# Kernel tuning notes

Measured on AMD Instinct MI355X. Metric: run time of the kernel, lower is better.

Reference implementation:

```python
import jax, jax.numpy as jnp
import numpy as np
import math

D = 1024
H = 16
DH = D // H
B = 4
NSEQ = 1024
NSEG = 2
EXP = 4


def layer_norm(x, w, b=None, eps=1e-5):
    mu = jnp.mean(x, axis=-1, keepdims=True)
    var = jnp.mean((x - mu) ** 2, axis=-1, keepdims=True)
    y = (x - mu) * jax.lax.rsqrt(var + eps) * w
    return y + b if b is not None else y


def apply_rope(x, positions):
    # x: [B, L, H, Dh]; ESM-style rotate-half RoPE
    dh = x.shape[-1]
    inv_freq = 1.0 / (10000.0 ** (jnp.arange(0, dh, 2, dtype=jnp.float32) / dh))
    freqs = positions.astype(jnp.float32)[:, None] * inv_freq[None, :]  # [L, Dh/2]
    emb = jnp.concatenate([freqs, freqs], axis=-1)  # [L, Dh]
    cos = jnp.cos(emb)[None, :, None, :]
    sin = jnp.sin(emb)[None, :, None, :]
    x1, x2 = jnp.split(x, 2, axis=-1)
    return x * cos + jnp.concatenate([-x2, x1], axis=-1) * sin


def timestep_embedding(timesteps, embedding_dim=256, max_len=10000):
    # timesteps: [N]
    ts = timesteps * max_len
    half = embedding_dim // 2
    emb = math.log(max_len) / (half - 1)
    freqs = jnp.exp(jnp.arange(half, dtype=jnp.float32) * -emb)
    e = ts.astype(jnp.float32)[:, None] * freqs[None, :]
    return jnp.concatenate([jnp.sin(e), jnp.cos(e)], axis=1)  # [N, 256]


def make_autoregressive_attn_mask(batch_mask, n_seg):
    b, n_res = batch_mask.shape
    L = (n_seg + 1) * n_res
    causal = jnp.tril(jnp.ones((L, L), dtype=bool))[None, None]  # [1,1,L,L]
    tiled = jnp.tile(batch_mask, (1, n_seg + 1)).astype(bool)  # [B, L]
    key_valid = tiled[:, None, None, :]
    q_valid = tiled[:, None, :, None]
    allowed = causal & key_valid & q_valid  # [B,1,L,L]
    first_edit = (batch_mask[:, None, :] * batch_mask[:, :, None]).astype(bool)
    allowed = allowed.at[:, 0, :n_res, :n_res].set(first_edit)
    return allowed


def setup_inputs() -> dict:
    key = jax.random.key(0)
    ks = jax.random.split(key, 32)
    s = 0.02
    p = lambda i, shape: jax.random.normal(ks[i], shape, dtype=jnp.float32) * s
    inp = {
        'x_seq': jax.random.normal(ks[0], (B, NSEQ, D), dtype=jnp.float32),
        'x_struc': jax.random.normal(ks[1], (B, 1, D), dtype=jnp.float32),
        'temp': jax.random.uniform(ks[2], (B, 1, 1), dtype=jnp.float32),
        'mask': jnp.ones((B, NSEQ), dtype=jnp.float32),
        'ln_qs_w': jnp.ones((D,), jnp.float32), 'ln_qs_b': jnp.zeros((D,), jnp.float32),
        'W_qkv_seq': p(3, (D, 3 * D)),
        'ln_qt_w': jnp.ones((D,), jnp.float32), 'ln_qt_b': jnp.zeros((D,), jnp.float32),
        'W_qkv_struc': p(4, (D, 3 * D)),
        'q_ln_seq_w': jnp.ones((D,), jnp.float32), 'k_ln_seq_w': jnp.ones((D,), jnp.float32),
        'q_ln_struc_w': jnp.ones((D,), jnp.float32), 'k_ln_struc_w': jnp.ones((D,), jnp.float32),
        'W_out_seq': p(5, (D, D)), 'W_out_struc': p(6, (D, D)),
        'temp_w1': p(7, (1, D)), 'temp_b1': jnp.zeros((D,), jnp.float32),
        'temp_w2': p(8, (D, D)), 'temp_b2': jnp.zeros((D,), jnp.float32),
        'T_w1': p(9, (256, D)), 'T_b1': jnp.zeros((D,), jnp.float32),
        'T_w2': p(10, (D, D)), 'T_b2': jnp.zeros((D,), jnp.float32),
        'ffn_seq_ln_w': jnp.ones((D,), jnp.float32), 'ffn_seq_ln_b': jnp.zeros((D,), jnp.float32),
        'ffn_seq_w1': p(11, (D, EXP * D)), 'ffn_seq_w2': p(12, (EXP * D, D)),
        'ffn_struc_ln_w': jnp.ones((D,), jnp.float32), 'ffn_struc_ln_b': jnp.zeros((D,), jnp.float32),
        'ffn_struc_w1': p(13, (D, EXP * D)), 'ffn_struc_w2': p(14, (EXP * D, D)),
        'T': 1,
    }
    return inp


def reference(x_seq, x_struc, temp, mask,
              ln_qs_w, ln_qs_b, W_qkv_seq,
              ln_qt_w, ln_qt_b, W_qkv_struc,
              q_ln_seq_w, k_ln_seq_w, q_ln_struc_w, k_ln_struc_w,
              W_out_seq, W_out_struc,
              temp_w1, temp_b1, temp_w2, temp_b2,
              T_w1, T_b1, T_w2, T_b2,
              ffn_seq_ln_w, ffn_seq_ln_b, ffn_seq_w1, ffn_seq_w2,
              ffn_struc_ln_w, ffn_struc_ln_b, ffn_struc_w1, ffn_struc_w2,
              T):
    b, n_seq, d = x_seq.shape
    n_seg, index = NSEG, 0  # index=0 prefill path

    # --- seq track QKV (index == 0 only) ---
    qkv_seq = layer_norm(x_seq, ln_qs_w, ln_qs_b) @ W_qkv_seq
    q_s, k_s, v_s = jnp.split(qkv_seq, 3, axis=-1)
    q_s = layer_norm(q_s, q_ln_seq_w)
    k_s = layer_norm(k_s, k_ln_seq_w)
    pos_seq = jnp.arange(n_seq)
    q_s = apply_rope(q_s.reshape(b, n_seq, H, DH), pos_seq).reshape(b, n_seq, d)
    k_s = apply_rope(k_s.reshape(b, n_seq, H, DH), pos_seq).reshape(b, n_seq, d)

    # --- struc track conditioning + QKV ---
    position_T = jnp.arange(n_seg, dtype=jnp.float32) * T / 100.0
    T_input = jnp.repeat(position_T, n_seq)[index:index + 1]  # [1]
    x_norm = layer_norm(x_struc, ln_qt_w, ln_qt_b)
    temp_e = jax.nn.silu(temp @ temp_w1 + temp_b1) @ temp_w2 + temp_b2  # [B,1,D]
    t_emb = timestep_embedding(T_input)  # [1,256]
    T_e = jax.nn.silu(t_emb @ T_w1 + T_b1) @ T_w2 + T_b2  # [1,D]
    x_mod = x_norm + temp_e + T_e[None, :, :]
    qkv_t = x_mod @ W_qkv_struc
    q_t, k_t, v_t = jnp.split(qkv_t, 3, axis=-1)
    q_t = layer_norm(q_t, q_ln_struc_w)
    k_t = layer_norm(k_t, k_ln_struc_w)
    pos_res = jnp.tile(jnp.arange(n_seq), n_seg)[index:index + 1]  # [1]
    q_t = apply_rope(q_t.reshape(b, 1, H, DH), pos_res).reshape(b, 1, d)
    k_t = apply_rope(k_t.reshape(b, 1, H, DH), pos_res).reshape(b, 1, d)

    # --- KV cache contents for index 0: [seq tokens, struc token] ---
    keys = jnp.concatenate([k_s, k_t], axis=1)    # [B, N_seq+1, D]
    values = jnp.concatenate([v_s, v_t], axis=1)
    queries = jnp.concatenate([q_s, q_t], axis=1)

    to_heads = lambda t: t.reshape(b, -1, H, DH).transpose(0, 2, 1, 3)  # b h s d
    qh, kh, vh = to_heads(queries), to_heads(keys), to_heads(values)

    allowed = make_autoregressive_attn_mask(mask, n_seg)  # [B,1,L,L]
    Lq = n_seq + index + 1
    attn_mask = allowed[:, :, :Lq, :Lq]

    scale = 1.0 / math.sqrt(DH)
    scores = jnp.einsum('bhqd,bhkd->bhqk', qh, kh) * scale
    scores = jnp.where(attn_mask, scores, -1e9)
    probs = jax.nn.softmax(scores, axis=-1)
    ctx = jnp.einsum('bhqk,bhkd->bhqd', probs, vh)
    ctx = ctx.transpose(0, 2, 1, 3).reshape(b, Lq, d)

    out_seq = ctx[:, :n_seq] @ W_out_seq
    out_struc = ctx[:, n_seq:] @ W_out_struc

    # residuals (scaling_factor = 1)
    x_seq = x_seq + out_seq
    x_struc = x_struc + out_struc

    # GELU FFNs (LN -> Linear -> GELU -> Linear, no bias)
    h_seq = jax.nn.gelu(layer_norm(x_seq, ffn_seq_ln_w, ffn_seq_ln_b) @ ffn_seq_w1, approximate=False) @ ffn_seq_w2
    x_seq = x_seq + h_seq
    h_struc = jax.nn.gelu(layer_norm(x_struc, ffn_struc_ln_w, ffn_struc_ln_b) @ ffn_struc_w1, approximate=False) @ ffn_struc_w2
    x_struc = x_struc + h_struc

    return (x_seq, x_struc)
```

## Files before the change

### kernel.cpp

```cpp
#include <hip/hip_runtime.h>

typedef __attribute__((ext_vector_type(8))) short short8;
typedef __attribute__((ext_vector_type(4))) float f32x4;
typedef __attribute__((ext_vector_type(4))) unsigned short us4;

#define DEV static __device__ __forceinline__

DEV float bf2f(unsigned short u){ union{unsigned u; float f;} v; v.u=((unsigned)u)<<16; return v.f; }
DEV unsigned short f2bf(float f){ union{float f; unsigned u;} v; v.f=f; unsigned r=v.u+0x7fffu+((v.u>>16)&1u); return (unsigned short)(r>>16); }
DEV float gelu_f(float x){ return 0.5f*x*(1.0f+erff(x*0.7071067811865475f)); }
DEV float silu_f(float x){ return x/(1.0f+__expf(-x)); }

DEV void gload16(const void* g, void* l){
  __builtin_amdgcn_global_load_lds((const __attribute__((address_space(1))) void*)g,
                                   (__attribute__((address_space(3))) void*)l, 16, 0, 0);
}

DEV void blk_reduce2(float &a, float &b){
  #pragma unroll
  for (int off=32; off>0; off>>=1){ a += __shfl_down(a,off); b += __shfl_down(b,off); }
  __shared__ float sa[4], sb[4];
  int w=threadIdx.x>>6;
  if((threadIdx.x&63)==0){ sa[w]=a; sb[w]=b; }
  __syncthreads();
  a=sa[0]+sa[1]+sa[2]+sa[3]; b=sb[0]+sb[1]+sb[2]+sb[3];
}

template<int OUTF32>
__global__ __launch_bounds__(256) void ln_rows(const float* __restrict__ x,
    const float* __restrict__ w, const float* __restrict__ bias, void* __restrict__ outp)
{
  int row=blockIdx.x, t=threadIdx.x;
  const float* xr = x + (size_t)row*1024;
  float4 v = *(const float4*)(xr + t*4);
  float s=v.x+v.y+v.z+v.w;
  float s2=v.x*v.x+v.y*v.y+v.z*v.z+v.w*v.w;
  blk_reduce2(s,s2);
  float mu=s*(1.0f/1024.0f);
  float rs=rsqrtf(s2*(1.0f/1024.0f)-mu*mu+1e-5f);
  int d0=t*4;
  const float* vp=(const float*)&v;
  float y[4];
  #pragma unroll
  for(int j=0;j<4;j++){ float bb = bias? bias[d0+j] : 0.0f; y[j]=(vp[j]-mu)*rs*w[d0+j]+bb; }
  if (OUTF32){
    float4 o; o.x=y[0];o.y=y[1];o.z=y[2];o.w=y[3];
    *(float4*)((float*)outp + (size_t)row*1024 + d0) = o;
  } else {
    us4 o;
    #pragma unroll
    for(int j=0;j<4;j++) o[j]=f2bf(y[j]);
    *(us4*)((unsigned short*)outp + (size_t)row*1024 + d0) = o;
  }
}

__global__ __launch_bounds__(256) void wtrans(const float* __restrict__ Bm,
    unsigned short* __restrict__ Bt, int K, int N)
{
  __shared__ float tile[32][33];
  int nb = blockIdx.x*32, kb = blockIdx.y*32;
  int tx = threadIdx.x&31, ty = threadIdx.x>>5;
  #pragma unroll
  for(int i=0;i<32;i+=8) tile[ty+i][tx] = Bm[(size_t)(kb+ty+i)*N + nb+tx];
  __syncthreads();
  #pragma unroll
  for(int i=0;i<32;i+=8) Bt[(size_t)(nb+ty+i)*K + kb+tx] = f2bf(tile[tx][ty+i]);
}

__global__ void rope_table(float* __restrict__ tab){
  int idx = blockIdx.x*256 + threadIdx.x;
  if (idx >= 1024*32) return;
  int pos = idx>>5, i = idx&31;
  float inv = exp2f(-(float)i * (13.287712379549449f/32.0f));
  float a = (float)pos*inv;
  tab[idx*2]   = cosf(a);
  tab[idx*2+1] = sinf(a);
}

__global__ __launch_bounds__(256) void qk_ln_rope(
    const unsigned short* __restrict__ qkv, const float* __restrict__ qw, const float* __restrict__ kw,
    const float* __restrict__ tab, unsigned short* __restrict__ qr, unsigned short* __restrict__ kr)
{
  __shared__ float lnr[1024];
  int row=blockIdx.x, part=blockIdx.y, t=threadIdx.x;
  const unsigned short* src = qkv + (size_t)row*3072 + part*1024 + t*4;
  us4 u = *(const us4*)src;
  float x[4];
  #pragma unroll
  for(int j=0;j<4;j++) x[j]=bf2f(u[j]);
  float s=x[0]+x[1]+x[2]+x[3];
  float s2=x[0]*x[0]+x[1]*x[1]+x[2]*x[2]+x[3]*x[3];
  blk_reduce2(s,s2);
  float mu=s*(1.0f/1024.0f);
  float rsg=rsqrtf(s2*(1.0f/1024.0f)-mu*mu+1e-5f);
  const float* w = part? kw : qw;
  int d0=t*4;
  #pragma unroll
  for(int j=0;j<4;j++) lnr[d0+j]=(x[j]-mu)*rsg*w[d0+j];
  __syncthreads();
  int n = row & 1023;
  unsigned short* dst = (part? kr: qr) + (size_t)row*1024 + d0;
  us4 o;
  #pragma unroll
  for(int j=0;j<4;j++){
    int d=d0+j, dh=d&63, fi=dh&31;
    float c=tab[(n*32+fi)*2], sn=tab[(n*32+fi)*2+1];
    float p=lnr[d^32];
    o[j]=f2bf(lnr[d]*c + ((dh<32)? -p : p)*sn);
  }
  *(us4*)dst = o;
}

template<int EPI>
__global__ __launch_bounds__(256) void gemm_bt(
    const unsigned short* __restrict__ A, int lda,
    const unsigned short* __restrict__ Bt, int ldb,
    int N, int K, void* Cout, const float* resp)
{
  __shared__ unsigned short As[8192];
  __shared__ unsigned short Bs[8192];
  const int t=threadIdx.x;
  int GX=gridDim.x, GY=gridDim.y, nwg=GX*GY;
  int m0, n0;
  if (!((GX&7) || (nwg&63))){
    int d = blockIdx.y*GX + blockIdx.x;
    int xcd = d&7, j = d>>3;
    int g = xcd*(nwg>>3) + j;
    int chunk = g>>6, local = g&63;
    int chunks_x = GX>>3;
    int cx = chunk%chunks_x, cy = chunk/chunks_x;
    n0 = (cx*8 + (local&7))*128;
    m0 = (cy*8 + (local>>3))*128;
  } else {
    m0 = blockIdx.y*128; n0 = blockIdx.x*128;
  }
  const int kofs = blockIdx.z*K;
  const int l=t&63, w=t>>6, lg=l>>4, lr=l&15;
  const int wm=(w>>1)*64, wn=(w&1)*64;
  const int srow=t>>3, sseg=(t&7)^(srow&7);
  const f32x4 z4 = {0.f,0.f,0.f,0.f};
  f32x4 acc[4][4];
  #pragma unroll
  for(int i=0;i<4;i++)
    #pragma unroll
    for(int j=0;j<4;j++) acc[i][j]=z4;
  for (int k0=0;k0<K;k0+=64){
    __syncthreads();
    #pragma unroll
    for(int i=0;i<4;i++){
      gload16(A  + (size_t)(m0+srow+i*32)*lda + kofs + k0 + sseg*8, As + w*512 + i*2048);
      gload16(Bt + (size_t)(n0+srow+i*32)*ldb + kofs + k0 + sseg*8, Bs + w*512 + i*2048);
    }
    __syncthreads();
    #pragma unroll
    for(int ks=0;ks<2;ks++){
      short8 a[4], bfr[4];
      #pragma unroll
      for(int m=0;m<4;m++){
        int row=wm+m*16+lr;
        a[m] = *(const short8*)&As[row*64 + ((ks*4+lg)^(row&7))*8];
      }
      #pragma unroll
      for(int n=0;n<4;n++){
        int row=wn+n*16+lr;
        bfr[n] = *(const short8*)&Bs[row*64 + ((ks*4+lg)^(row&7))*8];
      }
      #pragma unroll
      for(int m=0;m<4;m++)
        #pragma unroll
        for(int n=0;n<4;n++)
          acc[m][n] = __builtin_amdgcn_mfma_f32_16x16x32_bf16(a[m], bfr[n], acc[m][n], 0,0,0);
    }
  }
  #pragma unroll
  for(int m=0;m<4;m++){
    #pragma unroll
    for(int n=0;n<4;n++){
      #pragma unroll
      for(int r=0;r<4;r++){
        int row=m0+wm+m*16+lg*4+r, col=n0+wn+n*16+lr;
        size_t idx=(size_t)row*N+col;
        float v=acc[m][n][r];
        if (EPI==1){ ((float*)Cout)[idx] = v + resp[idx]; }
        else if (EPI==2){ ((unsigned short*)Cout)[idx] = f2bf(gelu_f(v)); }
        else if (EPI==3){ atomicAdd((float*)Cout + idx, v); }
        else { ((unsigned short*)Cout)[idx] = f2bf(v); }
      }
    }
  }
}

__global__ __launch_bounds__(256) void flash_seq(
    const unsigned short* __restrict__ qr, const unsigned short* __restrict__ kr,
    const unsigned short* __restrict__ qkv, unsigned short* __restrict__ ctx)
{
  __shared__ unsigned short Kt[64][72];
  __shared__ unsigned short Vt[64][72];
  __shared__ unsigned short Pl[4][32][72];
  const int t=threadIdx.x, w=t>>6, l=t&63, lg=l>>4, lr=l&15;
  const int bh=blockIdx.y, b=bh>>4, h=bh&15;
  const int q0=blockIdx.x*128;
  const f32x4 z4 = {0.f,0.f,0.f,0.f};
  short8 qf[2][2];
  #pragma unroll
  for(int mf=0;mf<2;mf++)
    #pragma unroll
    for(int ks=0;ks<2;ks++)
      qf[mf][ks] = *(const short8*)(qr + (size_t)(b*1024 + q0 + w*32 + mf*16 + lr)*1024 + h*64 + ks*32 + lg*8);
  f32x4 o[2][4];
  float m_[2][4], l_[2][4];
  #pragma unroll
  for(int mf=0;mf<2;mf++){
    #pragma unroll
    for(int nd=0;nd<4;nd++) o[mf][nd]=z4;
    #pragma unroll
    for(int r=0;r<4;r++){ m_[mf][r]=-1e30f; l_[mf][r]=0.f; }
  }
  for (int kv0=0;kv0<1024;kv0+=64){
    __syncthreads();
    #pragma unroll
    for(int i=0;i<2;i++){
      int idx=t+i*256, rr=idx>>3, seg=idx&7;
      *(short8*)&Kt[rr][seg*8] = *(const short8*)(kr + (size_t)(b*1024+kv0+rr)*1024 + h*64 + seg*8);
    }
    #pragma unroll
    for(int i=0;i<2;i++){
      int idx=t+i*256, rr=idx>>3, seg=idx&7;
      short8 vv = *(const short8*)(qkv + (size_t)(b*1024+kv0+rr)*3072 + 2048 + h*64 + seg*8);
      #pragma unroll
      for(int j=0;j<8;j++) Vt[seg*8+j][rr] = (unsigned short)vv[j];
    }
    __syncthreads();
    f32x4 s[2][4];
    #pragma unroll
    for(int mf=0;mf<2;mf++)
      #pragma unroll
      for(int nf=0;nf<4;nf++) s[mf][nf]=z4;
    #pragma unroll
    for(int ks=0;ks<2;ks++){
      #pragma unroll
      for(int nf=0;nf<4;nf++){
        short8 kf = *(const short8*)&Kt[nf*16+lr][ks*32+lg*8];
        s[0][nf] = __builtin_amdgcn_mfma_f32_16x16x32_bf16(qf[0][ks], kf, s[0][nf],0,0,0);
        s[1][nf] = __builtin_amdgcn_mfma_f32_16x16x32_bf16(qf[1][ks], kf, s[1][nf],0,0,0);
      }
    }
    #pragma unroll
    for(int mf=0;mf<2;mf++)
      #pragma unroll
      for(int nf=0;nf<4;nf++) s[mf][nf] = s[mf][nf]*0.125f;
    #pragma unroll
    for(int mf=0;mf<2;mf++){
      #pragma unroll
      for(int r=0;r<4;r++){
        float mx = fmaxf(fmaxf(s[mf][0][r],s[mf][1][r]),fmaxf(s[mf][2][r],s[mf][3][r]));
        #pragma unroll
        for(int off=8;off>0;off>>=1) mx = fmaxf(mx, __shfl_xor(mx,off));
        float mn = fmaxf(m_[mf][r], mx);
        float f  = __expf(m_[mf][r]-mn);
        float rs = 0.f;
        #pragma unroll
        for(int nf=0;nf<4;nf++){ float p=__expf(s[mf][nf][r]-mn); s[mf][nf][r]=p; rs+=p; }
        #pragma unroll
        for(int off=8;off>0;off>>=1) rs += __shfl_xor(rs,off);
        l_[mf][r]=l_[mf][r]*f+rs; m_[mf][r]=mn;
        #pragma unroll
        for(int nd=0;nd<4;nd++) o[mf][nd][r]*=f;
      }
    }
    #pragma unroll
    for(int mf=0;mf<2;mf++)
      #pragma unroll
      for(int nf=0;nf<4;nf++)
        #pragma unroll
        for(int r=0;r<4;r++)
          Pl[w][mf*16+lg*4+r][nf*16+lr] = f2bf(s[mf][nf][r]);
    #pragma unroll
    for(int ks2=0;ks2<2;ks2++){
      short8 pa0 = *(const short8*)&Pl[w][lr]   [ks2*32+lg*8];
      short8 pa1 = *(const short8*)&Pl[w][16+lr][ks2*32+lg*8];
      #pragma unroll
      for(int nd=0;nd<4;nd++){
        short8 vf = *(const short8*)&Vt[nd*16+lr][ks2*32+lg*8];
        o[0][nd] = __builtin_amdgcn_mfma_f32_16x16x32_bf16(pa0, vf, o[0][nd],0,0,0);
        o[1][nd] = __builtin_amdgcn_mfma_f32_16x16x32_bf16(pa1, vf, o[1][nd],0,0,0);
      }
    }
  }
  #pragma unroll
  for(int mf=0;mf<2;mf++){
    #pragma unroll
    for(int r=0;r<4;r++){
      float inv = 1.0f/l_[mf][r];
      #pragma unroll
      for(int nd=0;nd<4;nd++){
        ctx[(size_t)(b*1024 + q0 + w*32 + mf*16 + lg*4 + r)*1024 + h*64 + nd*16 + lr]
          = f2bf(o[mf][nd][r]*inv);
      }
    }
  }
}

__global__ __launch_bounds__(256) void struc_prep_a(const float* __restrict__ T_w1, float* __restrict__ sTacc){
  int j = blockIdx.x*256+threadIdx.x;
  float u=0.f;
  #pragma unroll
  for(int i=0;i<16;i++) u += T_w1[(size_t)(128+blockIdx.y*16+i)*1024 + j];
  atomicAdd(&sTacc[j], u);
}

__global__ __launch_bounds__(256) void struc_prep_b(const float* __restrict__ temp,
    const float* __restrict__ temp_w1, const float* __restrict__ temp_b1,
    const float* __restrict__ T_b1, const float* __restrict__ sTacc,
    float* __restrict__ sT, float* __restrict__ stemp)
{
  int j = blockIdx.x*256+threadIdx.x;
  sT[j] = silu_f(sTacc[j]+T_b1[j]);
  #pragma unroll
  for(int b=0;b<4;b++){ float z = temp[b]*temp_w1[j]+temp_b1[j]; stemp[b*1024+j]=silu_f(z); }
}

__global__ __launch_bounds__(256) void struc_xmod(const float* __restrict__ xs,
    const float* __restrict__ qtw, const float* __restrict__ qtb,
    const float* __restrict__ eacc, const float* __restrict__ tacc,
    const float* __restrict__ temp_b2, const float* __restrict__ T_b2, float* __restrict__ xmod)
{
  int b=blockIdx.x, t=threadIdx.x;
  float4 v = *(const float4*)(xs + (size_t)b*1024 + t*4);
  float s=v.x+v.y+v.z+v.w, s2=v.x*v.x+v.y*v.y+v.z*v.z+v.w*v.w;
  blk_reduce2(s,s2);
  float mu=s*(1.0f/1024.0f);
  float rs=rsqrtf(s2*(1.0f/1024.0f)-mu*mu+1e-5f);
  const float* vp=(const float*)&v;
  #pragma unroll
  for(int j=0;j<4;j++){
    int d=t*4+j;
    xmod[b*1024+d] = (vp[j]-mu)*rs*qtw[d] + qtb[d] + eacc[b*1024+d] + tacc[d] + T_b2[d] + temp_b2[d];
  }
}

template<int MR>
__global__ __launch_bounds__(256) void smallm_part(
    const float* __restrict__ A, const float* __restrict__ Bm,
    float* __restrict__ accp, int K, int N)
{
  __shared__ float As[MR][64];
  const int t=threadIdx.x;
  const int n = blockIdx.x*256 + t;
  const int k0 = blockIdx.y*64;
  if (t < MR*64){ int m=t>>6, kk=t&63; As[m][kk]=A[(size_t)m*K + k0+kk]; }
  __syncthreads();
  float acc[MR];
  #pragma unroll
  for(int m=0;m<MR;m++) acc[m]=0.f;
  #pragma unroll 8
  for(int kk=0;kk<64;kk++){
    float wv = Bm[(size_t)(k0+kk)*N + n];
    #pragma unroll
    for(int m=0;m<MR;m++) acc[m] += As[m][kk]*wv;
  }
  #pragma unroll
  for(int m=0;m<MR;m++) atomicAdd(&accp[(size_t)m*N + n], acc[m]);
}

__global__ __launch_bounds__(256) void gelu_vec(const float* __restrict__ in, float* __restrict__ out, int n){
  int i = blockIdx.x*256+threadIdx.x;
  if (i<n) out[i]=gelu_f(in[i]);
}

__global__ __launch_bounds__(256) void struc_qk_ln(float* qkv_t,
    const float* __restrict__ qw, const float* __restrict__ kw)
{
  int b=blockIdx.x>>1, part=blockIdx.x&1, t=threadIdx.x;
  float* xr = qkv_t + (size_t)b*3072 + part*1024;
  float4 v = *(const float4*)(xr + t*4);
  float s=v.x+v.y+v.z+v.w, s2=v.x*v.x+v.y*v.y+v.z*v.z+v.w*v.w;
  blk_reduce2(s,s2);
  float mu=s*(1.0f/1024.0f);
  float rsg=rsqrtf(s2*(1.0f/1024.0f)-mu*mu+1e-5f);
  const float* w = part? kw : qw;
  const float* vp=(const float*)&v;
  #pragma unroll
  for(int j=0;j<4;j++) xr[t*4+j]=(vp[j]-mu)*rsg*w[t*4+j];
}

__global__ __launch_bounds__(256) void struc_attn_part(
    const float* __restrict__ qkv_t, const unsigned short* __restrict__ kr,
    const unsigned short* __restrict__ qkv, float* __restrict__ part)
{
  __shared__ float qs[64];
  __shared__ float pb[4][64];
  const int bh=blockIdx.x, b=bh>>4, h=bh&15;
  const int t=threadIdx.x, w=t>>6, l=t&63;
  if (t<64) qs[t]=qkv_t[(size_t)b*3072 + h*64 + t];
  __syncthreads();
  const int key = blockIdx.y*256 + w*64 + l;
  const unsigned short* krow = kr + (size_t)(b*1024+key)*1024 + h*64;
  float s=0.f;
  #pragma unroll
  for(int j=0;j<8;j++){
    short8 kk = *(const short8*)(krow + j*8);
    #pragma unroll
    for(int e=0;e<8;e++) s += qs[j*8+e]*bf2f((unsigned short)kk[e]);
  }
  s *= 0.125f;
  float mx=s;
  #pragma unroll
  for(int off=32;off>0;off>>=1) mx=fmaxf(mx,__shfl_xor(mx,off));
  float p=__expf(s-mx);
  float ls=p;
  #pragma unroll
  for(int off=32;off>0;off>>=1) ls+=__shfl_xor(ls,off);
  pb[w][l]=p;
  const int k0 = blockIdx.y*256 + w*64;
  float cacc=0.f;
  for(int k2=0;k2<64;k2++)
    cacc += pb[w][k2]*bf2f(qkv[(size_t)(b*1024+k0+k2)*3072 + 2048 + h*64 + l]);
  float* pp = part + ((size_t)bh*16 + blockIdx.y*4 + w)*66;
  if(l==0){ pp[0]=mx; pp[1]=ls; }
  pp[2+l]=cacc;
}

__global__ __launch_bounds__(64) void struc_attn_comb(
    const float* __restrict__ part, const float* __restrict__ qkv_t, float* __restrict__ ctx_t)
{
  const int bh=blockIdx.x, b=bh>>4, h=bh&15, l=threadIdx.x;
  float M=-1e30f;
  #pragma unroll
  for(int i=0;i<16;i++) M=fmaxf(M, part[((size_t)bh*16+i)*66]);
  float lsum=0.f, cacc=0.f;
  #pragma unroll
  for(int i=0;i<16;i++){
    const float* pp = part + ((size_t)bh*16+i)*66;
    float f=__expf(pp[0]-M);
    lsum += pp[1]*f;
    cacc += pp[2+l]*f;
  }
  float qd=qkv_t[(size_t)b*3072 + h*64 + l];
  float kd=qkv_t[(size_t)b*3072 + 1024 + h*64 + l];
  float prod=qd*kd;
  #pragma unroll
  for(int off=32;off>0;off>>=1) prod+=__shfl_xor(prod,off);
  float st=prod*0.125f;
  float M2=fmaxf(M,st), fA=__expf(M-M2), pt=__expf(st-M2);
  cacc = cacc*fA + pt*qkv_t[(size_t)b*3072 + 2048 + h*64 + l];
  lsum = lsum*fA + pt;
  ctx_t[(size_t)b*1024 + h*64 + l] = cacc/lsum;
}

extern "C" void kernel_launch(void* const* d_in, const int* in_sizes, int n_in,
                              void* d_out, int out_size, void* d_ws, size_t ws_size,
                              hipStream_t stream){
  const float* x_seq    = (const float*)d_in[0];
  const float* x_struc  = (const float*)d_in[1];
  const float* temp     = (const float*)d_in[2];
  const float* ln_qs_w  = (const float*)d_in[4];
  const float* ln_qs_b  = (const float*)d_in[5];
  const float* W_qkv_seq= (const float*)d_in[6];
  const float* ln_qt_w  = (const float*)d_in[7];
  const float* ln_qt_b  = (const float*)d_in[8];
  const float* W_qkv_st = (const float*)d_in[9];
  const float* q_ln_seq_w=(const float*)d_in[10];
  const float* k_ln_seq_w=(const float*)d_in[11];
  const float* q_ln_st_w= (const float*)d_in[12];
  const float* k_ln_st_w= (const float*)d_in[13];
  const float* W_out_seq= (const float*)d_in[14];
  const float* W_out_st = (const float*)d_in[15];
  const float* temp_w1  = (const float*)d_in[16];
  const float* temp_b1  = (const float*)d_in[17];
  const float* temp_w2  = (const float*)d_in[18];
  const float* temp_b2  = (const float*)d_in[19];
  const float* T_w1     = (const float*)d_in[20];
  const float* T_b1     = (const float*)d_in[21];
  const float* T_w2     = (const float*)d_in[22];
  const float* T_b2     = (const float*)d_in[23];
  const float* ffn_s_ln_w=(const float*)d_in[24];
  const float* ffn_s_ln_b=(const float*)d_in[25];
  const float* ffn_s_w1 = (const float*)d_in[26];
  const float* ffn_s_w2 = (const float*)d_in[27];
  const float* ffn_t_ln_w=(const float*)d_in[28];
  const float* ffn_t_ln_b=(const float*)d_in[29];
  const float* ffn_t_w1 = (const float*)d_in[30];
  const float* ffn_t_w2 = (const float*)d_in[31];

  char* ws = (char*)d_ws;
  unsigned short* xn   = (unsigned short*)(ws + 0);
  unsigned short* qkv  = (unsigned short*)(ws + 8388608);
  unsigned short* qr   = (unsigned short*)(ws + 33554432);
  unsigned short* kr   = (unsigned short*)(ws + 41943040);
  unsigned short* ctx  = (unsigned short*)(ws + 50331648);
  float* tab   = (float*)(ws + 58720256);
  char* sm = ws + 58982400;
  float* sT    = (float*)(sm + 0);
  float* stemp = (float*)(sm + 4096);
  float* tacc  = (float*)(sm + 20544);
  float* eacc  = (float*)(sm + 24640);
  float* xmod  = (float*)(sm + 41024);
  float* qkvt  = (float*)(sm + 57408);
  float* ctxt  = (float*)(sm + 106560);
  float* xsn   = (float*)(sm + 122944);
  float* hs    = (float*)(sm + 139328);
  float* hsacc = (float*)(sm + 204864);
  float* part  = (float*)(sm + 270400);
  float* sTacc = (float*)(sm + 540800);
  unsigned short* wqkvT = (unsigned short*)(ws + 50331648);
  unsigned short* woutT = (unsigned short*)(ws + 33554432);
  unsigned short* ffn1T = (unsigned short*)(ws + 41943040);
  unsigned short* ffn2T = (unsigned short*)(ws + 50331648);
  unsigned short* hbuf = qkv;
  float* outf = (float*)d_out;
  float* out_tail = outf + 4194304;

  ln_rows<0><<<4096,256,0,stream>>>(x_seq, ln_qs_w, ln_qs_b, xn);
  wtrans<<<dim3(96,32),256,0,stream>>>(W_qkv_seq, wqkvT, 1024, 3072);
  rope_table<<<128,256,0,stream>>>(tab);
  gemm_bt<0><<<dim3(24,32),256,0,stream>>>(xn, 1024, wqkvT, 1024, 3072, 1024, qkv, nullptr);
  qk_ln_rope<<<dim3(4096,2),256,0,stream>>>(qkv, q_ln_seq_w, k_ln_seq_w, tab, qr, kr);
  flash_seq<<<dim3(8,64),256,0,stream>>>(qr, kr, qkv, ctx);
  hipMemsetAsync(sTacc, 0, 1024*4, stream);
  hipMemsetAsync(tacc, 0, 1024*4, stream);
  hipMemsetAsync(eacc, 0, 4096*4, stream);
  hipMemsetAsync(qkvt, 0, 12288*4, stream);
  struc_prep_a<<<dim3(4,8),256,0,stream>>>(T_w1, sTacc);
  struc_prep_b<<<4,256,0,stream>>>(temp, temp_w1, temp_b1, T_b1, sTacc, sT, stemp);
  smallm_part<1><<<dim3(4,16),256,0,stream>>>(sT, T_w2, tacc, 1024, 1024);
  smallm_part<4><<<dim3(4,16),256,0,stream>>>(stemp, temp_w2, eacc, 1024, 1024);
  struc_xmod<<<4,256,0,stream>>>(x_struc, ln_qt_w, ln_qt_b, eacc, tacc, temp_b2, T_b2, xmod);
  smallm_part<4><<<dim3(12,16),256,0,stream>>>(xmod, W_qkv_st, qkvt, 1024, 3072);
  struc_qk_ln<<<8,256,0,stream>>>(qkvt, q_ln_st_w, k_ln_st_w);
  struc_attn_part<<<dim3(64,4),256,0,stream>>>(qkvt, kr, qkv, part);
  struc_attn_comb<<<64,64,0,stream>>>(part, qkvt, ctxt);
  wtrans<<<dim3(32,32),256,0,stream>>>(W_out_seq, woutT, 1024, 1024);
  hipMemcpyAsync(outf, x_seq, (size_t)4194304*4, hipMemcpyDeviceToDevice, stream);
  gemm_bt<3><<<dim3(8,32,2),256,0,stream>>>(ctx, 1024, woutT, 1024, 1024, 512, outf, nullptr);
  hipMemcpyAsync(out_tail, x_struc, 4096*4, hipMemcpyDeviceToDevice, stream);
  smallm_part<4><<<dim3(4,16),256,0,stream>>>(ctxt, W_out_st, out_tail, 1024, 1024);
  ln_rows<0><<<4096,256,0,stream>>>(outf, ffn_s_ln_w, ffn_s_ln_b, xn);
  wtrans<<<dim3(128,32),256,0,stream>>>(ffn_s_w1, ffn1T, 1024, 4096);
  gemm_bt<2><<<dim3(32,32),256,0,stream>>>(xn, 1024, ffn1T, 1024, 4096, 1024, hbuf, nullptr);
  wtrans<<<dim3(32,128),256,0,stream>>>(ffn_s_w2, ffn2T, 4096, 1024);
  gemm_bt<3><<<dim3(8,32,4),256,0,stream>>>(hbuf, 4096, ffn2T, 4096, 1024, 1024, outf, nullptr);
  ln_rows<1><<<4,256,0,stream>>>(out_tail, ffn_t_ln_w, ffn_t_ln_b, xsn);
  hipMemsetAsync(hsacc, 0, 16384*4, stream);
  smallm_part<4><<<dim3(16,16),256,0,stream>>>(xsn, ffn_t_w1, hsacc, 1024, 4096);
  gelu_vec<<<64,256,0,stream>>>(hsacc, hs, 16384);
  smallm_part<4><<<dim3(4,64),256,0,stream>>>(hs, ffn_t_w2, out_tail, 4096, 1024);
  (void)in_sizes; (void)n_in; (void)out_size; (void)ws_size;
}
```

Measured before the change: 490.4 us.

## Read K and pre-transposed V directly from global in flash attention, swizzle P, remap blocks to XCDs

Adds a vtrans kernel that writes V transposed into a spare buffer, so the flash kernel can load K and V MFMA operands straight from global (L2) instead of staging them through shared memory with two barriers per tile. The P scratch tile drops its padding and uses an XOR swizzle to avoid LDS bank conflicts. Block indices are remapped so that blocks sharing a batch-head pair land on the same XCD for L2 reuse. The cost is an extra transpose kernel and uncoalesced, latency-bound global loads in the inner loop.

```diff
diff --git a/kernel.cpp b/kernel.cpp
--- a/kernel.cpp
+++ b/kernel.cpp
@@ -65,6 +65,19 @@
   __syncthreads();
   #pragma unroll
   for(int i=0;i<32;i+=8) Bt[(size_t)(nb+ty+i)*K + kb+tx] = f2bf(tile[tx][ty+i]);
+}
+
+__global__ __launch_bounds__(256) void vtrans(const unsigned short* __restrict__ qkv,
+    unsigned short* __restrict__ vT)
+{
+  __shared__ unsigned short tile[32][33];
+  int d0 = blockIdx.x*32, tk0 = blockIdx.y*32, b = blockIdx.z;
+  int tx = threadIdx.x&31, ty = threadIdx.x>>5;
+  #pragma unroll
+  for(int i=0;i<32;i+=8) tile[ty+i][tx] = qkv[(size_t)(b*1024+tk0+ty+i)*3072 + 2048 + d0+tx];
+  __syncthreads();
+  #pragma unroll
+  for(int i=0;i<32;i+=8) vT[(size_t)(b*1024+d0+ty+i)*1024 + tk0+tx] = tile[tx][ty+i];
 }
 
 __global__ void rope_table(float* __restrict__ tab){
@@ -192,14 +205,15 @@
 
 __global__ __launch_bounds__(256) void flash_seq(
     const unsigned short* __restrict__ qr, const unsigned short* __restrict__ kr,
-    const unsigned short* __restrict__ qkv, unsigned short* __restrict__ ctx)
-{
-  __shared__ unsigned short Kt[64][72];
-  __shared__ unsigned short Vt[64][72];
-  __shared__ unsigned short Pl[4][32][72];
+    const unsigned short* __restrict__ vT, unsigned short* __restrict__ ctx)
+{
+  __shared__ unsigned short Pl[4][32][64];
   const int t=threadIdx.x, w=t>>6, l=t&63, lg=l>>4, lr=l&15;
-  const int bh=blockIdx.y, b=bh>>4, h=bh&15;
-  const int q0=blockIdx.x*128;
+  int d = blockIdx.y*gridDim.x + blockIdx.x;
+  int xcd = d&7;
+  int g = xcd*64 + (d>>3);
+  const int bh = g>>3, b = bh>>4, h = bh&15;
+  const int q0 = (g&7)*128;
   const f32x4 z4 = {0.f,0.f,0.f,0.f};
   short8 qf[2][2];
   #pragma unroll
@@ -217,20 +231,6 @@
     for(int r=0;r<4;r++){ m_[mf][r]=-1e30f; l_[mf][r]=0.f; }
   }
   for (int kv0=0;kv0<1024;kv0+=64){
-    __syncthreads();
-    #pragma unroll
-    for(int i=0;i<2;i++){
-      int idx=t+i*256, rr=idx>>3, seg=idx&7;
-      *(short8*)&Kt[rr][seg*8] = *(const short8*)(kr + (size_t)(b*1024+kv0+rr)*1024 + h*64 + seg*8);
-    }
-    #pragma unroll
-    for(int i=0;i<2;i++){
-      int idx=t+i*256, rr=idx>>3, seg=idx&7;
-      short8 vv = *(const short8*)(qkv + (size_t)(b*1024+kv0+rr)*3072 + 2048 + h*64 + seg*8);
-      #pragma unroll
-      for(int j=0;j<8;j++) Vt[seg*8+j][rr] = (unsigned short)vv[j];
-    }
-    __syncthreads();
     f32x4 s[2][4];
     #pragma unroll
     for(int mf=0;mf<2;mf++)
@@ -240,7 +240,7 @@
     for(int ks=0;ks<2;ks++){
       #pragma unroll
       for(int nf=0;nf<4;nf++){
-        short8 kf = *(const short8*)&Kt[nf*16+lr][ks*32+lg*8];
+        short8 kf = *(const short8*)(kr + (size_t)(b*1024+kv0+nf*16+lr)*1024 + h*64 + ks*32 + lg*8);
         s[0][nf] = __builtin_amdgcn_mfma_f32_16x16x32_bf16(qf[0][ks], kf, s[0][nf],0,0,0);
         s[1][nf] = __builtin_amdgcn_mfma_f32_16x16x32_bf16(qf[1][ks], kf, s[1][nf],0,0,0);
       }
@@ -273,15 +273,18 @@
       #pragma unroll
       for(int nf=0;nf<4;nf++)
         #pragma unroll
-        for(int r=0;r<4;r++)
-          Pl[w][mf*16+lg*4+r][nf*16+lr] = f2bf(s[mf][nf][r]);
+        for(int r=0;r<4;r++){
+          int prow = mf*16+lg*4+r;
+          int col = (((nf*2+(lr>>3)) ^ (prow&7))<<3) + (lr&7);
+          Pl[w][prow][col] = f2bf(s[mf][nf][r]);
+        }
     #pragma unroll
     for(int ks2=0;ks2<2;ks2++){
-      short8 pa0 = *(const short8*)&Pl[w][lr]   [ks2*32+lg*8];
-      short8 pa1 = *(const short8*)&Pl[w][16+lr][ks2*32+lg*8];
+      short8 pa0 = *(const short8*)&Pl[w][lr]   [((ks2*4+lg)^(lr&7))<<3];
+      short8 pa1 = *(const short8*)&Pl[w][16+lr][((ks2*4+lg)^(lr&7))<<3];
       #pragma unroll
       for(int nd=0;nd<4;nd++){
-        short8 vf = *(const short8*)&Vt[nd*16+lr][ks2*32+lg*8];
+        short8 vf = *(const short8*)(vT + (size_t)(b*1024 + h*64 + nd*16+lr)*1024 + kv0 + ks2*32 + lg*8);
         o[0][nd] = __builtin_amdgcn_mfma_f32_16x16x32_bf16(pa0, vf, o[0][nd],0,0,0);
         o[1][nd] = __builtin_amdgcn_mfma_f32_16x16x32_bf16(pa1, vf, o[1][nd],0,0,0);
       }
@@ -507,6 +510,7 @@
   unsigned short* woutT = (unsigned short*)(ws + 33554432);
   unsigned short* ffn1T = (unsigned short*)(ws + 41943040);
   unsigned short* ffn2T = (unsigned short*)(ws + 50331648);
+  unsigned short* vT   = xn;
   unsigned short* hbuf = qkv;
   float* outf = (float*)d_out;
   float* out_tail = outf + 4194304;
@@ -515,8 +519,9 @@
   wtrans<<<dim3(96,32),256,0,stream>>>(W_qkv_seq, wqkvT, 1024, 3072);
   rope_table<<<128,256,0,stream>>>(tab);
   gemm_bt<0><<<dim3(24,32),256,0,stream>>>(xn, 1024, wqkvT, 1024, 3072, 1024, qkv, nullptr);
+  vtrans<<<dim3(32,32,4),256,0,stream>>>(qkv, vT);
   qk_ln_rope<<<dim3(4096,2),256,0,stream>>>(qkv, q_ln_seq_w, k_ln_seq_w, tab, qr, kr);
-  flash_seq<<<dim3(8,64),256,0,stream>>>(qr, kr, qkv, ctx);
+  flash_seq<<<dim3(8,64),256,0,stream>>>(qr, kr, vT, ctx);
   hipMemsetAsync(sTacc, 0, 1024*4, stream);
   hipMemsetAsync(tacc, 0, 1024*4, stream);
   hipMemsetAsync(eacc, 0, 4096*4, stream);
```

New measurement: 484.6 us. No clear change (-1.2%).
